# Optimization experiments

Measured on AMD Instinct MI355X. Metric: run time of the kernel, lower is better.

The kernel has to match this reference:

```python
import jax, jax.numpy as jnp
import numpy as np

NUM_TOKENS = 16384
NUM_HEADS = 8
HEAD_SIZE = 128
NUM_BLOCKS = 4096
BLOCK_SIZE = 16
NUM_SLOTS = NUM_BLOCKS * BLOCK_SIZE


def setup_inputs() -> dict:
    key = jax.random.key(0)
    k1, k2, k3, k4, k5 = jax.random.split(key, 5)
    # Unique, in-range slots (random permutation) so the scatter is deterministic.
    slot_mapping = jax.random.permutation(k5, NUM_SLOTS)[:NUM_TOKENS].astype(jnp.int64)
    return {
        "key": jax.random.normal(k1, (NUM_TOKENS, NUM_HEADS, HEAD_SIZE), dtype=jnp.float32),
        "value": jax.random.normal(k2, (NUM_TOKENS, NUM_HEADS, HEAD_SIZE), dtype=jnp.float32),
        "key_cache": jax.random.normal(k3, (NUM_BLOCKS, BLOCK_SIZE, NUM_HEADS, HEAD_SIZE), dtype=jnp.float32),
        "value_cache": jax.random.normal(k4, (NUM_BLOCKS, BLOCK_SIZE, NUM_HEADS, HEAD_SIZE), dtype=jnp.float32),
        "slot_mapping": slot_mapping,
        "k_scale": jnp.ones((1,), dtype=jnp.float32),
        "v_scale": jnp.ones((1,), dtype=jnp.float32),
    }


def reference(key, value, key_cache, value_cache, slot_mapping, k_scale, v_scale):
    # kv_cache_dtype='auto' in the torch Model, so FP8_KV_CACHE is False and
    # k_scale/v_scale are never applied. The op is a pure paged scatter:
    #   cache[slot // block_size, slot % block_size] = token  (skip slot < 0)
    num_blocks, block_size = key_cache.shape[0], key_cache.shape[1]
    num_slots = num_blocks * block_size
    # View caches as flat slot-major [num_slots, heads, head_size].
    kc_flat = key_cache.reshape(num_slots, *key_cache.shape[2:])
    vc_flat = value_cache.reshape(num_slots, *value_cache.shape[2:])
    # Redirect negative slots out-of-range; mode='drop' skips those writes.
    safe_slot = jnp.where(slot_mapping < 0, num_slots, slot_mapping)
    kc_flat = kc_flat.at[safe_slot].set(key, mode="drop")
    vc_flat = vc_flat.at[safe_slot].set(value, mode="drop")
    return (kc_flat.reshape(key_cache.shape), vc_flat.reshape(value_cache.shape))
```

## Files before the change

kernel.cpp:

```cpp
#include <hip/hip_runtime.h>

#define NUM_TOKENS   16384
#define NUM_HEADS    8
#define HEAD_SIZE    128
#define NUM_BLOCKS   4096
#define BLOCK_SIZE_  16
#define SLOT_ELEMS   (NUM_HEADS * HEAD_SIZE)
#define SLOT_VEC4    (SLOT_ELEMS / 4)
#define NUM_SLOTS    (NUM_BLOCKS * BLOCK_SIZE_)
#define CACHE_ELEMS  ((long)NUM_SLOTS * SLOT_ELEMS)


__global__ void build_inverse_kernel(const int* __restrict__ slot_mapping,
                                     int* __restrict__ inv) {
    int t = blockIdx.x * blockDim.x + threadIdx.x;
    if (t < NUM_TOKENS) {
        int s = slot_mapping[t];
        if (s >= 0) inv[s] = t;
    }
}

__global__ void fused_cache_kernel(const float4* __restrict__ key,
                                   const float4* __restrict__ value,
                                   const float4* __restrict__ kc,
                                   const float4* __restrict__ vc,
                                   const int* __restrict__ inv,
                                   float4* __restrict__ ok,
                                   float4* __restrict__ ov) {
    int slot = blockIdx.x;
    int tid  = threadIdx.x;
    int token = inv[slot];
    long dst = (long)slot * SLOT_VEC4 + tid;
    if (token >= 0) {
        long src = (long)token * SLOT_VEC4 + tid;
        ok[dst] = key[src];
        ov[dst] = value[src];
    } else {
        ok[dst] = kc[dst];
        ov[dst] = vc[dst];
    }
}


__global__ void copy_cache_kernel(const float4* __restrict__ kc,
                                  const float4* __restrict__ vc,
                                  float4* __restrict__ ok,
                                  float4* __restrict__ ov,
                                  long n4) {
    long i = (long)blockIdx.x * blockDim.x + threadIdx.x;
    long stride = (long)gridDim.x * blockDim.x;
    for (; i < n4; i += stride) {
        ok[i] = kc[i];
        ov[i] = vc[i];
    }
}

__global__ void scatter_kv_kernel(const float4* __restrict__ key,
                                  const float4* __restrict__ value,
                                  const int* __restrict__ slot_mapping,
                                  float4* __restrict__ ok,
                                  float4* __restrict__ ov) {
    int token = blockIdx.x;
    int slot = slot_mapping[token];
    if (slot < 0) return;
    int tid = threadIdx.x;
    long src = (long)token * SLOT_VEC4 + tid;
    long dst = (long)slot  * SLOT_VEC4 + tid;
    ok[dst] = key[src];
    ov[dst] = value[src];
}

extern "C" void kernel_launch(void* const* d_in, const int* in_sizes, int n_in,
                              void* d_out, int out_size, void* d_ws, size_t ws_size,
                              hipStream_t stream) {
    const float* key   = (const float*)d_in[0];
    const float* value = (const float*)d_in[1];
    const float* kc    = (const float*)d_in[2];
    const float* vc    = (const float*)d_in[3];
    const int*   slots = (const int*)d_in[4];

    float* ok = (float*)d_out;
    float* ov = ok + CACHE_ELEMS;

    if (ws_size >= (size_t)NUM_SLOTS * sizeof(int)) {
        int* inv = (int*)d_ws;
        hipMemsetAsync(inv, 0xFF, NUM_SLOTS * sizeof(int), stream);
        build_inverse_kernel<<<(NUM_TOKENS + 255) / 256, 256, 0, stream>>>(slots, inv);
        fused_cache_kernel<<<NUM_SLOTS, 256, 0, stream>>>(
            (const float4*)key, (const float4*)value,
            (const float4*)kc, (const float4*)vc, inv,
            (float4*)ok, (float4*)ov);
    } else {
        long n4 = CACHE_ELEMS / 4;
        copy_cache_kernel<<<2048, 256, 0, stream>>>(
            (const float4*)kc, (const float4*)vc, (float4*)ok, (float4*)ov, n4);
        scatter_kv_kernel<<<NUM_TOKENS, 256, 0, stream>>>(
            (const float4*)key, (const float4*)value, slots, (float4*)ok, (float4*)ov);
    }
}
```

Measured before the change: 203.3 us.

## Use persistent warp-per-slot loop with separate key/value block halves

Replaces the one-block-per-slot launch with a fixed grid of 2048 blocks. The first half handles the key cache and the second half the value cache, and each 64-lane wavefront loops over slots with a grid stride, copying a full slot as four float4 loads and stores per lane. The slot's token index is read once per wavefront through readfirstlane. This cuts block-launch overhead and puts more loads in flight per thread, at the cost of a loop and possible load imbalance across wavefronts.

```diff
diff --git a/kernel.cpp b/kernel.cpp
--- a/kernel.cpp
+++ b/kernel.cpp
@@ -10,6 +10,7 @@
 #define NUM_SLOTS    (NUM_BLOCKS * BLOCK_SIZE_)
 #define CACHE_ELEMS  ((long)NUM_SLOTS * SLOT_ELEMS)
 
+#define HALF_BLOCKS  1024
 
 __global__ void build_inverse_kernel(const int* __restrict__ slot_mapping,
                                      int* __restrict__ inv) {
@@ -27,17 +28,39 @@
                                    const int* __restrict__ inv,
                                    float4* __restrict__ ok,
                                    float4* __restrict__ ov) {
-    int slot = blockIdx.x;
-    int tid  = threadIdx.x;
-    int token = inv[slot];
-    long dst = (long)slot * SLOT_VEC4 + tid;
-    if (token >= 0) {
-        long src = (long)token * SLOT_VEC4 + tid;
-        ok[dst] = key[src];
-        ov[dst] = value[src];
-    } else {
-        ok[dst] = kc[dst];
-        ov[dst] = vc[dst];
+    bool is_v = blockIdx.x >= HALF_BLOCKS;
+    const float4* __restrict__ src_tok   = is_v ? value : key;
+    const float4* __restrict__ src_cache = is_v ? vc    : kc;
+    float4* __restrict__       dst       = is_v ? ov    : ok;
+
+    int halfBlk = blockIdx.x - (is_v ? HALF_BLOCKS : 0);
+    int gw   = (halfBlk * blockDim.x + threadIdx.x) >> 6;
+    int lane = threadIdx.x & 63;
+    const int NW = HALF_BLOCKS * 256 / 64;
+
+    for (int slot = gw; slot < NUM_SLOTS; slot += NW) {
+        int token = __builtin_amdgcn_readfirstlane(inv[slot]);
+        long db = ((long)slot << 8) + lane;
+        if (token >= 0) {
+            long sb = ((long)token << 8) + lane;
+            float4 r0 = src_tok[sb +   0];
+            float4 r1 = src_tok[sb +  64];
+            float4 r2 = src_tok[sb + 128];
+            float4 r3 = src_tok[sb + 192];
+            dst[db +   0] = r0;
+            dst[db +  64] = r1;
+            dst[db + 128] = r2;
+            dst[db + 192] = r3;
+        } else {
+            float4 r0 = src_cache[db +   0];
+            float4 r1 = src_cache[db +  64];
+            float4 r2 = src_cache[db + 128];
+            float4 r3 = src_cache[db + 192];
+            dst[db +   0] = r0;
+            dst[db +  64] = r1;
+            dst[db + 128] = r2;
+            dst[db + 192] = r3;
+        }
     }
 }
 
@@ -86,7 +109,7 @@
         int* inv = (int*)d_ws;
         hipMemsetAsync(inv, 0xFF, NUM_SLOTS * sizeof(int), stream);
         build_inverse_kernel<<<(NUM_TOKENS + 255) / 256, 256, 0, stream>>>(slots, inv);
-        fused_cache_kernel<<<NUM_SLOTS, 256, 0, stream>>>(
+        fused_cache_kernel<<<2 * HALF_BLOCKS, 256, 0, stream>>>(
             (const float4*)key, (const float4*)value,
             (const float4*)kc, (const float4*)vc, inv,
             (float4*)ok, (float4*)ov);
```

Result: slower. 216.1 us (+6.3%).

## Make fused cache kernel persistent with per-wave slot loops split by K/V

Applied to the files above, without the earlier changes.

Replaces the one-block-per-slot launch (65536 blocks) with a fixed grid of 2048 blocks. Each half of the grid handles either the key or the value cache. Each 64-lane wave loops over 16 strided slots, prefetches their inverse-map entries up front, and copies a slot as four float4 loads then four stores per lane. This cuts block launch and scheduling overhead and gives more memory-level parallelism per thread. The cost is fewer resident waves and longer per-wave serial work, which could leave bandwidth unused if occupancy drops.

```diff
diff --git a/kernel.cpp b/kernel.cpp
--- a/kernel.cpp
+++ b/kernel.cpp
@@ -10,6 +10,9 @@
 #define NUM_SLOTS    (NUM_BLOCKS * BLOCK_SIZE_)
 #define CACHE_ELEMS  ((long)NUM_SLOTS * SLOT_ELEMS)
 
+#define HALF_BLOCKS     1024
+#define WAVES_PER_HALF  (HALF_BLOCKS * 256 / 64)
+#define SLOTS_PER_WAVE  (NUM_SLOTS / WAVES_PER_HALF)
 
 __global__ void build_inverse_kernel(const int* __restrict__ slot_mapping,
                                      int* __restrict__ inv) {
@@ -20,24 +23,43 @@
     }
 }
 
-__global__ void fused_cache_kernel(const float4* __restrict__ key,
-                                   const float4* __restrict__ value,
-                                   const float4* __restrict__ kc,
-                                   const float4* __restrict__ vc,
-                                   const int* __restrict__ inv,
-                                   float4* __restrict__ ok,
-                                   float4* __restrict__ ov) {
-    int slot = blockIdx.x;
-    int tid  = threadIdx.x;
-    int token = inv[slot];
-    long dst = (long)slot * SLOT_VEC4 + tid;
-    if (token >= 0) {
-        long src = (long)token * SLOT_VEC4 + tid;
-        ok[dst] = key[src];
-        ov[dst] = value[src];
-    } else {
-        ok[dst] = kc[dst];
-        ov[dst] = vc[dst];
+__global__ __launch_bounds__(256)
+void fused_cache_kernel(const float4* __restrict__ key,
+                        const float4* __restrict__ value,
+                        const float4* __restrict__ kc,
+                        const float4* __restrict__ vc,
+                        const int* __restrict__ inv,
+                        float4* __restrict__ ok,
+                        float4* __restrict__ ov) {
+    bool is_v = blockIdx.x >= HALF_BLOCKS;
+    const float4* __restrict__ src_tok   = is_v ? value : key;
+    const float4* __restrict__ src_cache = is_v ? vc    : kc;
+    float4* __restrict__       dst       = is_v ? ov    : ok;
+
+    int halfBlk = is_v ? (blockIdx.x - HALF_BLOCKS) : blockIdx.x;
+    int gw   = (halfBlk * 256 + (int)threadIdx.x) >> 6;
+    int lane = threadIdx.x & 63;
+
+    int tok[SLOTS_PER_WAVE];
+#pragma unroll
+    for (int k = 0; k < SLOTS_PER_WAVE; ++k)
+        tok[k] = inv[gw + k * WAVES_PER_HALF];
+
+#pragma unroll 4
+    for (int k = 0; k < SLOTS_PER_WAVE; ++k) {
+        int  slot = gw + k * WAVES_PER_HALF;
+        long db   = ((long)slot << 8) + lane;
+        const float4* __restrict__ src =
+            (tok[k] >= 0) ? (src_tok + (((long)tok[k] << 8) + lane))
+                          : (src_cache + db);
+        float4 r0 = src[0];
+        float4 r1 = src[64];
+        float4 r2 = src[128];
+        float4 r3 = src[192];
+        dst[db +   0] = r0;
+        dst[db +  64] = r1;
+        dst[db + 128] = r2;
+        dst[db + 192] = r3;
     }
 }
 
@@ -86,7 +108,7 @@
         int* inv = (int*)d_ws;
         hipMemsetAsync(inv, 0xFF, NUM_SLOTS * sizeof(int), stream);
         build_inverse_kernel<<<(NUM_TOKENS + 255) / 256, 256, 0, stream>>>(slots, inv);
-        fused_cache_kernel<<<NUM_SLOTS, 256, 0, stream>>>(
+        fused_cache_kernel<<<2 * HALF_BLOCKS, 256, 0, stream>>>(
             (const float4*)key, (const float4*)value,
             (const float4*)kc, (const float4*)vc, inv,
             (float4*)ok, (float4*)ov);
```

Result: slower. 215.1 us (+5.8%).

## Split fused cache kernel into hole-copy and scatter kernels with nontemporal loads/stores

Applied to the files above, without the earlier changes.

Replaces the single per-slot fused kernel, which gathered token data through the inverse map, with two kernels. One copies only the unoccupied cache slots and the other scatters tokens directly by slot_mapping. All global loads and stores now use nontemporal builtins so streaming data bypasses cache retention. This adds a kernel launch and makes the gather indirection a scatter, and the hole-copy kernel still launches one block per slot, with early exit for filled slots.

```diff
diff --git a/kernel.cpp b/kernel.cpp
--- a/kernel.cpp
+++ b/kernel.cpp
@@ -10,6 +10,14 @@
 #define NUM_SLOTS    (NUM_BLOCKS * BLOCK_SIZE_)
 #define CACHE_ELEMS  ((long)NUM_SLOTS * SLOT_ELEMS)
 
+typedef float f4_t __attribute__((ext_vector_type(4)));
+__device__ __forceinline__ void nt_store(float4* p, float4 v) {
+    __builtin_nontemporal_store(*(f4_t*)&v, (f4_t*)p);
+}
+__device__ __forceinline__ float4 nt_load(const float4* p) {
+    f4_t v = __builtin_nontemporal_load((const f4_t*)p);
+    return *(float4*)&v;
+}
 
 __global__ void build_inverse_kernel(const int* __restrict__ slot_mapping,
                                      int* __restrict__ inv) {
@@ -20,25 +28,37 @@
     }
 }
 
-__global__ void fused_cache_kernel(const float4* __restrict__ key,
-                                   const float4* __restrict__ value,
-                                   const float4* __restrict__ kc,
-                                   const float4* __restrict__ vc,
-                                   const int* __restrict__ inv,
-                                   float4* __restrict__ ok,
-                                   float4* __restrict__ ov) {
+__global__ __launch_bounds__(256)
+void scatter_kv_kernel(const float4* __restrict__ key,
+                       const float4* __restrict__ value,
+                       const int* __restrict__ slot_mapping,
+                       float4* __restrict__ ok,
+                       float4* __restrict__ ov) {
+    int token = blockIdx.x;
+    int slot = slot_mapping[token];
+    if (slot < 0) return;
+    int tid = threadIdx.x;
+    long src = (long)token * SLOT_VEC4 + tid;
+    long dst = (long)slot  * SLOT_VEC4 + tid;
+    float4 rk = nt_load(key + src);
+    float4 rv = nt_load(value + src);
+    nt_store(ok + dst, rk);
+    nt_store(ov + dst, rv);
+}
+
+__global__ __launch_bounds__(256)
+void copy_holes_kernel(const float4* __restrict__ kc,
+                       const float4* __restrict__ vc,
+                       const int* __restrict__ inv,
+                       float4* __restrict__ ok,
+                       float4* __restrict__ ov) {
     int slot = blockIdx.x;
-    int tid  = threadIdx.x;
-    int token = inv[slot];
-    long dst = (long)slot * SLOT_VEC4 + tid;
-    if (token >= 0) {
-        long src = (long)token * SLOT_VEC4 + tid;
-        ok[dst] = key[src];
-        ov[dst] = value[src];
-    } else {
-        ok[dst] = kc[dst];
-        ov[dst] = vc[dst];
-    }
+    if (inv[slot] >= 0) return;
+    long i = (long)slot * SLOT_VEC4 + threadIdx.x;
+    float4 rk = nt_load(kc + i);
+    float4 rv = nt_load(vc + i);
+    nt_store(ok + i, rk);
+    nt_store(ov + i, rv);
 }
 
 
@@ -53,21 +73,6 @@
         ok[i] = kc[i];
         ov[i] = vc[i];
     }
-}
-
-__global__ void scatter_kv_kernel(const float4* __restrict__ key,
-                                  const float4* __restrict__ value,
-                                  const int* __restrict__ slot_mapping,
-                                  float4* __restrict__ ok,
-                                  float4* __restrict__ ov) {
-    int token = blockIdx.x;
-    int slot = slot_mapping[token];
-    if (slot < 0) return;
-    int tid = threadIdx.x;
-    long src = (long)token * SLOT_VEC4 + tid;
-    long dst = (long)slot  * SLOT_VEC4 + tid;
-    ok[dst] = key[src];
-    ov[dst] = value[src];
 }
 
 extern "C" void kernel_launch(void* const* d_in, const int* in_sizes, int n_in,
@@ -86,10 +91,10 @@
         int* inv = (int*)d_ws;
         hipMemsetAsync(inv, 0xFF, NUM_SLOTS * sizeof(int), stream);
         build_inverse_kernel<<<(NUM_TOKENS + 255) / 256, 256, 0, stream>>>(slots, inv);
-        fused_cache_kernel<<<NUM_SLOTS, 256, 0, stream>>>(
-            (const float4*)key, (const float4*)value,
-            (const float4*)kc, (const float4*)vc, inv,
-            (float4*)ok, (float4*)ov);
+        copy_holes_kernel<<<NUM_SLOTS, 256, 0, stream>>>(
+            (const float4*)kc, (const float4*)vc, inv, (float4*)ok, (float4*)ov);
+        scatter_kv_kernel<<<NUM_TOKENS, 256, 0, stream>>>(
+            (const float4*)key, (const float4*)value, slots, (float4*)ok, (float4*)ov);
     } else {
         long n4 = CACHE_ELEMS / 4;
         copy_cache_kernel<<<2048, 256, 0, stream>>>(
```

Result: no change. 200.8 us (median of 2 runs) (-1.2%).
